# Kernel optimization log

Hardware: AMD Instinct MI355X
Metric: run time of the kernel (lower is better)

## Reference

```python
import jax, jax.numpy as jnp
import numpy as np

B, C_IN, H, W = 4, 8, 128, 128
C_OUT, KH, KW = 16, 5, 5


def _patches(img, kh, kw):
    """Extract valid sliding windows. img: [B,C,H,W] -> [B, C, kh*kw, Ho, Wo]."""
    b, c, h, w = img.shape
    ho, wo = h - kh + 1, w - kw + 1
    views = [img[:, :, i:i + ho, j:j + wo] for i in range(kh) for j in range(kw)]
    return jnp.stack(views, axis=2)  # small fixed loop over kh*kw offsets


def setup_inputs() -> dict:
    key = jax.random.key(0)
    k1, k2 = jax.random.split(key)
    img = jax.random.normal(k1, (B, C_IN, H, W), dtype=jnp.float32)
    kernel = jax.random.normal(k2, (C_OUT, C_IN, KH, KW), dtype=jnp.float32)
    return {"img": img, "kernel": kernel}


def reference(img, kernel):
    # Max-plus (tropical) semifield convolution, kind='conv':
    # out[b,o,y,x] = max_{c,i,j} ( img[b,c,y+i,x+j] + kernel_flipped[o,c,i,j] )
    kflip = kernel[:, :, ::-1, ::-1]            # true convolution: flip kernel spatially
    o, c, kh, kw = kflip.shape
    p = _patches(img, kh, kw)                    # [B, C, K, Ho, Wo], K = kh*kw
    b, _, k, ho, wo = p.shape
    p = p.reshape(b, c * k, ho * wo)             # [B, R, P]   R = C*K reduction dim
    wmat = kflip.reshape(o, c * k)               # [O, R]
    # tropical matmul: broadcast-add then max-reduce over R
    out = jnp.max(wmat[None, :, :, None] + p[:, None, :, :], axis=2)  # [B, O, P]
    return out.reshape(b, o, ho, wo)
```

## Files before the change

### kernel.cpp

```cpp
#include <hip/hip_runtime.h>
#include <math.h>

#define B_  4
#define CI  8
#define HH  128
#define WW  128
#define CO  16
#define KH  5
#define KW  5
#define HO  124
#define WO  124

#define TX  32
#define TY  8
#define THREADS 512

__global__ __launch_bounds__(THREADS)
void maxplus_conv2(const float* __restrict__ img,
                   const float* __restrict__ kern,
                   float* __restrict__ out)
{
    __shared__ __align__(16) float ilds[CI][TY + KH - 1][TX + KW - 1];

    const int tid = threadIdx.x;
    const int x0  = blockIdx.x * TX;
    const int y0  = blockIdx.y * TY;
    const int b   = blockIdx.z;

    const float* imgb = img + (size_t)b * CI * HH * WW;
    for (int idx = tid; idx < CI * 12 * 36; idx += THREADS) {
        const int col = idx % 36;
        const int t   = idx / 36;
        const int r   = t % 12;
        const int c   = t / 12;
        const int gy = y0 + r, gx = x0 + col;
        float v = -INFINITY;
        if (gy < HH && gx < WW) v = imgb[(c * HH + gy) * WW + gx];
        ilds[c][r][col] = v;
    }
    __syncthreads();

    const int tx = tid & 7;
    const int ty = (tid >> 3) & 7;
    const int o0 = __builtin_amdgcn_readfirstlane((tid >> 6) << 1);

    float acc[4][2];
    #pragma unroll
    for (int p = 0; p < 4; ++p) {
        acc[p][0] = -INFINITY;
        acc[p][1] = -INFINITY;
    }

    #pragma unroll 1
    for (int cp = 0; cp < CI / 2; ++cp) {
        const int c0 = cp * 2, c1 = cp * 2 + 1;
        #pragma unroll
        for (int i = 0; i < KH; ++i) {
            const float* p0 = &ilds[c0][ty + i][tx * 4];
            const float* p1 = &ilds[c1][ty + i][tx * 4];
            const float4 a0 = *(const float4*)(p0);
            const float4 a1 = *(const float4*)(p0 + 4);
            const float4 b0 = *(const float4*)(p1);
            const float4 b1 = *(const float4*)(p1 + 4);
            const float v0[8] = {a0.x, a0.y, a0.z, a0.w, a1.x, a1.y, a1.z, a1.w};
            const float v1[8] = {b0.x, b0.y, b0.z, b0.w, b1.x, b1.y, b1.z, b1.w};
            #pragma unroll
            for (int j = 0; j < KW; ++j) {
                const int wi = (4 - i) * KW + (4 - j);
                const float w00 = kern[(o0 * CI + c0) * (KH * KW) + wi];
                const float w01 = kern[((o0 + 1) * CI + c0) * (KH * KW) + wi];
                const float w10 = kern[(o0 * CI + c1) * (KH * KW) + wi];
                const float w11 = kern[((o0 + 1) * CI + c1) * (KH * KW) + wi];
                #pragma unroll
                for (int p = 0; p < 4; ++p) {
                    acc[p][0] = fmaxf(fmaxf(acc[p][0], v0[p + j] + w00), v1[p + j] + w10);
                    acc[p][1] = fmaxf(fmaxf(acc[p][1], v0[p + j] + w01), v1[p + j] + w11);
                }
            }
        }
    }

    const int y = y0 + ty;
    const int x = x0 + tx * 4;
    if (y < HO && x < WO) {
        #pragma unroll
        for (int q = 0; q < 2; ++q) {
            const int o = o0 + q;
            float4 st;
            st.x = acc[0][q]; st.y = acc[1][q]; st.z = acc[2][q]; st.w = acc[3][q];
            *(float4*)&out[(((size_t)b * CO + o) * HO + y) * WO + x] = st;
        }
    }
}

extern "C" void kernel_launch(void* const* d_in, const int* in_sizes, int n_in,
                              void* d_out, int out_size, void* d_ws, size_t ws_size,
                              hipStream_t stream)
{
    const float* img  = (const float*)d_in[0];
    const float* kern = (const float*)d_in[1];
    float* out = (float*)d_out;

    dim3 grid((WO + TX - 1) / TX, (HO + TY - 1) / TY, B_);
    dim3 block(THREADS);
    maxplus_conv2<<<grid, block, 0, stream>>>(img, kern, out);
}
```

Measured before the change: 16.08 us.

## Vectorize LDS tile fill, preload per-channel weights, and tree-reduce max chains

The global-to-LDS tile load now uses float4 accesses in two unrolled iterations instead of a scalar strided loop. The channel loop processes one channel at a time and preloads its 2x25 weights into registers up front, so there are no per-tap scalar loads inside the compute loop. Each row's five tap sums are combined with a shallower max tree, which shortens the dependency chain on the accumulators. The cost is higher register pressure from the 50 preloaded weights at 512 threads per block. The float4 fill also relies on 16-byte aligned global addresses, which holds because the tile origin and row width are multiples of four.

Measured after the change: 15.34 us. 1.05x faster.

```diff
diff --git a/kernel.cpp b/kernel.cpp
--- a/kernel.cpp
+++ b/kernel.cpp
@@ -16,7 +16,7 @@
 #define THREADS 512
 
 __global__ __launch_bounds__(THREADS)
-void maxplus_conv2(const float* __restrict__ img,
+void maxplus_conv3(const float* __restrict__ img,
                    const float* __restrict__ kern,
                    float* __restrict__ out)
 {
@@ -28,15 +28,24 @@
     const int b   = blockIdx.z;
 
     const float* imgb = img + (size_t)b * CI * HH * WW;
-    for (int idx = tid; idx < CI * 12 * 36; idx += THREADS) {
-        const int col = idx % 36;
-        const int t   = idx / 36;
-        const int r   = t % 12;
-        const int c   = t / 12;
-        const int gy = y0 + r, gx = x0 + col;
-        float v = -INFINITY;
-        if (gy < HH && gx < WW) v = imgb[(c * HH + gy) * WW + gx];
-        ilds[c][r][col] = v;
+    #pragma unroll
+    for (int it = 0; it < 2; ++it) {
+        const int idx = tid + it * THREADS;
+        if (idx < 864) {
+            const int c   = idx / 108;
+            const int rem = idx - c * 108;
+            const int r   = rem / 9;
+            const int f4  = rem - r * 9;
+            const int gy = y0 + r;
+            const int gx = x0 + f4 * 4;
+            float4 v;
+            if (gy < HH && gx < WW) {
+                v = *(const float4*)&imgb[(c * HH + gy) * WW + gx];
+            } else {
+                v.x = v.y = v.z = v.w = -INFINITY;
+            }
+            *(float4*)&ilds[c][r][f4 * 4] = v;
+        }
     }
     __syncthreads();
 
@@ -44,38 +53,47 @@
     const int ty = (tid >> 3) & 7;
     const int o0 = __builtin_amdgcn_readfirstlane((tid >> 6) << 1);
 
-    float acc[4][2];
+    const float* w0p = kern + (size_t)o0 * (CI * KH * KW);
+    const float* w1p = w0p + CI * KH * KW;
+
+    float2 acc[4];
     #pragma unroll
-    for (int p = 0; p < 4; ++p) {
-        acc[p][0] = -INFINITY;
-        acc[p][1] = -INFINITY;
-    }
+    for (int p = 0; p < 4; ++p) { acc[p].x = -INFINITY; acc[p].y = -INFINITY; }
 
     #pragma unroll 1
-    for (int cp = 0; cp < CI / 2; ++cp) {
-        const int c0 = cp * 2, c1 = cp * 2 + 1;
+    for (int c = 0; c < CI; ++c) {
+        float w0[25], w1[25];
+        #pragma unroll
+        for (int t = 0; t < 25; ++t) {
+            w0[t] = w0p[c * 25 + t];
+            w1[t] = w1p[c * 25 + t];
+        }
+        float4 va[5], vb[5];
         #pragma unroll
         for (int i = 0; i < KH; ++i) {
-            const float* p0 = &ilds[c0][ty + i][tx * 4];
-            const float* p1 = &ilds[c1][ty + i][tx * 4];
-            const float4 a0 = *(const float4*)(p0);
-            const float4 a1 = *(const float4*)(p0 + 4);
-            const float4 b0 = *(const float4*)(p1);
-            const float4 b1 = *(const float4*)(p1 + 4);
-            const float v0[8] = {a0.x, a0.y, a0.z, a0.w, a1.x, a1.y, a1.z, a1.w};
-            const float v1[8] = {b0.x, b0.y, b0.z, b0.w, b1.x, b1.y, b1.z, b1.w};
+            const float* vp = &ilds[c][ty + i][tx * 4];
+            va[i] = *(const float4*)vp;
+            vb[i] = *(const float4*)(vp + 4);
+        }
+        #pragma unroll
+        for (int i = 0; i < KH; ++i) {
+            const float v[8] = {va[i].x, va[i].y, va[i].z, va[i].w,
+                                vb[i].x, vb[i].y, vb[i].z, vb[i].w};
             #pragma unroll
-            for (int j = 0; j < KW; ++j) {
-                const int wi = (4 - i) * KW + (4 - j);
-                const float w00 = kern[(o0 * CI + c0) * (KH * KW) + wi];
-                const float w01 = kern[((o0 + 1) * CI + c0) * (KH * KW) + wi];
-                const float w10 = kern[(o0 * CI + c1) * (KH * KW) + wi];
-                const float w11 = kern[((o0 + 1) * CI + c1) * (KH * KW) + wi];
+            for (int p = 0; p < 4; ++p) {
+                float2 T[5];
                 #pragma unroll
-                for (int p = 0; p < 4; ++p) {
-                    acc[p][0] = fmaxf(fmaxf(acc[p][0], v0[p + j] + w00), v1[p + j] + w10);
-                    acc[p][1] = fmaxf(fmaxf(acc[p][1], v0[p + j] + w01), v1[p + j] + w11);
+                for (int j = 0; j < KW; ++j) {
+                    const int wi = (4 - i) * KW + (4 - j);
+                    T[j].x = v[p + j] + w0[wi];
+                    T[j].y = v[p + j] + w1[wi];
                 }
+                const float m0x = fmaxf(fmaxf(T[0].x, T[1].x), T[2].x);
+                const float m1x = fmaxf(T[3].x, T[4].x);
+                acc[p].x = fmaxf(fmaxf(acc[p].x, m0x), m1x);
+                const float m0y = fmaxf(fmaxf(T[0].y, T[1].y), T[2].y);
+                const float m1y = fmaxf(T[3].y, T[4].y);
+                acc[p].y = fmaxf(fmaxf(acc[p].y, m0y), m1y);
             }
         }
     }
@@ -83,13 +101,11 @@
     const int y = y0 + ty;
     const int x = x0 + tx * 4;
     if (y < HO && x < WO) {
-        #pragma unroll
-        for (int q = 0; q < 2; ++q) {
-            const int o = o0 + q;
-            float4 st;
-            st.x = acc[0][q]; st.y = acc[1][q]; st.z = acc[2][q]; st.w = acc[3][q];
-            *(float4*)&out[(((size_t)b * CO + o) * HO + y) * WO + x] = st;
-        }
+        float4 s0, s1;
+        s0.x = acc[0].x; s0.y = acc[1].x; s0.z = acc[2].x; s0.w = acc[3].x;
+        s1.x = acc[0].y; s1.y = acc[1].y; s1.z = acc[2].y; s1.w = acc[3].y;
+        *(float4*)&out[(((size_t)b * CO + o0) * HO + y) * WO + x] = s0;
+        *(float4*)&out[(((size_t)b * CO + o0 + 1) * HO + y) * WO + x] = s1;
     }
 }
 
@@ -103,5 +119,5 @@
 
     dim3 grid((WO + TX - 1) / TX, (HO + TY - 1) / TY, B_);
     dim3 block(THREADS);
-    maxplus_conv2<<<grid, block, 0, stream>>>(img, kern, out);
+    maxplus_conv3<<<grid, block, 0, stream>>>(img, kern, out);
 }
```
